# Performance work log

Measured on AMD Instinct MI355X. Metric: run time of the kernel, lower is better.

Reference implementation:

```python
import jax, jax.numpy as jnp
import numpy as np

CLASS_NUM = 19
B, H, W = 8, 512, 512


def setup_inputs() -> dict:
    key = jax.random.key(0)
    k1, k2 = jax.random.split(key)
    inp = jax.random.normal(k1, (B, CLASS_NUM, H, W), dtype=jnp.float32)
    target = jax.random.randint(k2, (B, H, W), 0, CLASS_NUM, dtype=jnp.int32)
    return {"input": inp, "target": target, "class_num": CLASS_NUM}


def reference(input, target, class_num):
    # argmax over channel dim (original permutes NCHW -> NHWC then argmax last dim;
    # equivalent to argmax over axis=1 of NCHW)
    pred = jnp.argmax(input, axis=1)                     # [B, H, W] int
    category = (class_num * target.astype(jnp.int32) + pred.astype(jnp.int32)).reshape(-1)
    # fused histogram scatter replacing the original O(N * class_num^2) equality loop
    confusion = jnp.zeros(class_num * class_num, dtype=jnp.int32).at[category].add(1)
    return confusion.reshape(class_num, class_num)
```

## Files before the change

kernel.cpp:

```cpp
#include <hip/hip_runtime.h>

#define CLASS_NUM 19
#define NBINS (CLASS_NUM * CLASS_NUM)
#define HW (512 * 512)
#define NPIX (8 * HW)
#define NVEC (NPIX / 4)
#define HWV (HW / 4)

__global__ void zero_out_kernel(int* __restrict__ out) {
    int t = threadIdx.x;
    if (t < NBINS) out[t] = 0;
}

__global__ __launch_bounds__(512, 4) void confusion_kernel(
    const float4* __restrict__ in,
    const int4*  __restrict__ tgt,
    int* __restrict__ out)
{
    __shared__ int hist[NBINS];
    for (int i = threadIdx.x; i < NBINS; i += 512) hist[i] = 0;
    __syncthreads();

    const int g   = blockIdx.x * 512 + threadIdx.x;
    const int b   = g >> 16;
    const int hwv = g & (HWV - 1);
    const float4* p = in + (size_t)b * (CLASS_NUM * HWV) + hwv;

    float4 v[CLASS_NUM];
    #pragma unroll
    for (int c = 0; c < CLASS_NUM; ++c) v[c] = p[(size_t)c * HWV];

    float4 best = v[0];
    int bx = 0, by = 0, bz = 0, bw = 0;
    #pragma unroll
    for (int c = 1; c < CLASS_NUM; ++c) {
        if (v[c].x > best.x) { best.x = v[c].x; bx = c; }
        if (v[c].y > best.y) { best.y = v[c].y; by = c; }
        if (v[c].z > best.z) { best.z = v[c].z; bz = c; }
        if (v[c].w > best.w) { best.w = v[c].w; bw = c; }
    }

    const int4 t = tgt[g];
    atomicAdd(&hist[t.x * CLASS_NUM + bx], 1);
    atomicAdd(&hist[t.y * CLASS_NUM + by], 1);
    atomicAdd(&hist[t.z * CLASS_NUM + bz], 1);
    atomicAdd(&hist[t.w * CLASS_NUM + bw], 1);

    __syncthreads();
    for (int i = threadIdx.x; i < NBINS; i += 512) {
        int h = hist[i];
        if (h) atomicAdd(&out[i], h);
    }
}

extern "C" void kernel_launch(void* const* d_in, const int* in_sizes, int n_in,
                              void* d_out, int out_size, void* d_ws, size_t ws_size,
                              hipStream_t stream) {
    const float4* in  = (const float4*)d_in[0];
    const int4*   tgt = (const int4*)d_in[1];
    int* out = (int*)d_out;

    zero_out_kernel<<<1, 512, 0, stream>>>(out);

    confusion_kernel<<<NVEC / 512, 512, 0, stream>>>(in, tgt, out);
}
```

Measured before the change: 230.1 us.

## Process two float4 quads per thread with nontemporal streaming loads

Each thread now handles two float4 pixel groups, which halves the block count and the per-block shared-histogram setup and flush. Input loads use nontemporal builtins and are interleaved with a branchless select/fmax argmax instead of first being gathered into a 19-entry register array. Target loads are issued early. In exchange, each block flushes more atomics to its shared histogram, and the interleaved loads can lower memory-level parallelism compared with loading all classes up front.

```diff
diff --git a/kernel.cpp b/kernel.cpp
--- a/kernel.cpp
+++ b/kernel.cpp
@@ -6,48 +6,67 @@
 #define NPIX (8 * HW)
 #define NVEC (NPIX / 4)
 #define HWV (HW / 4)
+#define QPT 2
+#define TPB 512
+#define TILE (TPB * QPT)
+#define NBLK (NVEC / TILE)
+
+typedef float f4 __attribute__((ext_vector_type(4)));
 
 __global__ void zero_out_kernel(int* __restrict__ out) {
     int t = threadIdx.x;
     if (t < NBINS) out[t] = 0;
 }
 
-__global__ __launch_bounds__(512, 4) void confusion_kernel(
-    const float4* __restrict__ in,
-    const int4*  __restrict__ tgt,
+__global__ __launch_bounds__(TPB, 4) void confusion_kernel(
+    const f4*   __restrict__ in,
+    const int4* __restrict__ tgt,
     int* __restrict__ out)
 {
     __shared__ int hist[NBINS];
-    for (int i = threadIdx.x; i < NBINS; i += 512) hist[i] = 0;
+    for (int i = threadIdx.x; i < NBINS; i += TPB) hist[i] = 0;
     __syncthreads();
 
-    const int g   = blockIdx.x * 512 + threadIdx.x;
-    const int b   = g >> 16;
-    const int hwv = g & (HWV - 1);
-    const float4* p = in + (size_t)b * (CLASS_NUM * HWV) + hwv;
+    const int g0 = blockIdx.x * TILE + threadIdx.x;
+    const int g1 = g0 + TPB;
+    const int b  = g0 >> 16;
+    const int h0 = g0 & (HWV - 1);
+    const f4* p0 = in + (size_t)b * (CLASS_NUM * HWV) + h0;
+    const f4* p1 = p0 + TPB;
 
-    float4 v[CLASS_NUM];
-    #pragma unroll
-    for (int c = 0; c < CLASS_NUM; ++c) v[c] = p[(size_t)c * HWV];
+    const int4 t0 = tgt[g0];
+    const int4 t1 = tgt[g1];
 
-    float4 best = v[0];
-    int bx = 0, by = 0, bz = 0, bw = 0;
+    f4 best0 = __builtin_nontemporal_load(p0);
+    f4 best1 = __builtin_nontemporal_load(p1);
+    int i0x = 0, i0y = 0, i0z = 0, i0w = 0;
+    int i1x = 0, i1y = 0, i1z = 0, i1w = 0;
+
     #pragma unroll
     for (int c = 1; c < CLASS_NUM; ++c) {
-        if (v[c].x > best.x) { best.x = v[c].x; bx = c; }
-        if (v[c].y > best.y) { best.y = v[c].y; by = c; }
-        if (v[c].z > best.z) { best.z = v[c].z; bz = c; }
-        if (v[c].w > best.w) { best.w = v[c].w; bw = c; }
+        f4 v0 = __builtin_nontemporal_load(p0 + (size_t)c * HWV);
+        f4 v1 = __builtin_nontemporal_load(p1 + (size_t)c * HWV);
+        i0x = (v0.x > best0.x) ? c : i0x;  best0.x = fmaxf(best0.x, v0.x);
+        i0y = (v0.y > best0.y) ? c : i0y;  best0.y = fmaxf(best0.y, v0.y);
+        i0z = (v0.z > best0.z) ? c : i0z;  best0.z = fmaxf(best0.z, v0.z);
+        i0w = (v0.w > best0.w) ? c : i0w;  best0.w = fmaxf(best0.w, v0.w);
+        i1x = (v1.x > best1.x) ? c : i1x;  best1.x = fmaxf(best1.x, v1.x);
+        i1y = (v1.y > best1.y) ? c : i1y;  best1.y = fmaxf(best1.y, v1.y);
+        i1z = (v1.z > best1.z) ? c : i1z;  best1.z = fmaxf(best1.z, v1.z);
+        i1w = (v1.w > best1.w) ? c : i1w;  best1.w = fmaxf(best1.w, v1.w);
     }
 
-    const int4 t = tgt[g];
-    atomicAdd(&hist[t.x * CLASS_NUM + bx], 1);
-    atomicAdd(&hist[t.y * CLASS_NUM + by], 1);
-    atomicAdd(&hist[t.z * CLASS_NUM + bz], 1);
-    atomicAdd(&hist[t.w * CLASS_NUM + bw], 1);
+    atomicAdd(&hist[t0.x * CLASS_NUM + i0x], 1);
+    atomicAdd(&hist[t0.y * CLASS_NUM + i0y], 1);
+    atomicAdd(&hist[t0.z * CLASS_NUM + i0z], 1);
+    atomicAdd(&hist[t0.w * CLASS_NUM + i0w], 1);
+    atomicAdd(&hist[t1.x * CLASS_NUM + i1x], 1);
+    atomicAdd(&hist[t1.y * CLASS_NUM + i1y], 1);
+    atomicAdd(&hist[t1.z * CLASS_NUM + i1z], 1);
+    atomicAdd(&hist[t1.w * CLASS_NUM + i1w], 1);
 
     __syncthreads();
-    for (int i = threadIdx.x; i < NBINS; i += 512) {
+    for (int i = threadIdx.x; i < NBINS; i += TPB) {
         int h = hist[i];
         if (h) atomicAdd(&out[i], h);
     }
@@ -56,11 +75,11 @@
 extern "C" void kernel_launch(void* const* d_in, const int* in_sizes, int n_in,
                               void* d_out, int out_size, void* d_ws, size_t ws_size,
                               hipStream_t stream) {
-    const float4* in  = (const float4*)d_in[0];
-    const int4*   tgt = (const int4*)d_in[1];
+    const f4*   in  = (const f4*)d_in[0];
+    const int4* tgt = (const int4*)d_in[1];
     int* out = (int*)d_out;
 
     zero_out_kernel<<<1, 512, 0, stream>>>(out);
 
-    confusion_kernel<<<NVEC / 512, 512, 0, stream>>>(in, tgt, out);
+    confusion_kernel<<<NBLK, TPB, 0, stream>>>(in, tgt, out);
 }
```

New measurement: 217.5 us. -5.5%, faster.
